# Kernel tuning notes

Measured on AMD Instinct MI355X. Metric: run time of the kernel, lower is better.

Reference implementation:

```python
import jax, jax.numpy as jnp
import numpy as np

S, B, D, H, FF = 1024, 8, 512, 8, 2048
HD = D // H
ALPHA, BETA = 0.5, 0.5
EPS = 1e-5


def setup_inputs() -> dict:
    key = jax.random.key(0)
    ks = jax.random.split(key, 12)
    rn = lambda k, sh, sc=0.02: jax.random.normal(k, sh, dtype=jnp.float32) * sc
    ln = jnp.stack([jnp.ones(D), jnp.zeros(D), jnp.ones(D), jnp.zeros(D)]).astype(jnp.float32)
    return {
        "src": rn(ks[0], (S, B, D), 1.0),
        "src_depth": rn(ks[1], (S, B, D), 1.0),
        "pos": rn(ks[2], (S, B, D), 1.0),
        "attn_w_img": rn(ks[3], (4, D, D)),
        "attn_b_img": jnp.zeros((4, D), jnp.float32),
        "attn_w_dpt": rn(ks[4], (4, D, D)),
        "attn_b_dpt": jnp.zeros((4, D), jnp.float32),
        "ffn_w1_img": rn(ks[5], (FF, D)),
        "ffn_b1_img": jnp.zeros((FF,), jnp.float32),
        "ffn_w2_img": rn(ks[6], (D, FF)),
        "ffn_b2_img": jnp.zeros((D,), jnp.float32),
        "ffn_w1_dpt": rn(ks[7], (FF, D)),
        "ffn_b1_dpt": jnp.zeros((FF,), jnp.float32),
        "ffn_w2_dpt": rn(ks[8], (D, FF)),
        "ffn_b2_dpt": jnp.zeros((D,), jnp.float32),
        "ln_img": ln,
        "ln_dpt": ln,
    }


def _layer_norm(x, g, b):
    m = jnp.mean(x, axis=-1, keepdims=True)
    v = jnp.var(x, axis=-1, keepdims=True)  # biased, matches torch LayerNorm
    return (x - m) * jax.lax.rsqrt(v + EPS) * g + b


def _heads(t, W, b):  # [B,S,D] x [D,D] -> [B,H,S,hd]  (torch Linear: y = x W^T + b)
    y = jnp.einsum('bsd,ed->bse', t, W) + b
    return y.reshape(B, S, H, HD).transpose(0, 2, 1, 3)


def _forward(src, src_depth, pos, attn_w_img, attn_b_img, attn_w_dpt, attn_b_dpt,
             ffn_w1_img, ffn_b1_img, ffn_w2_img, ffn_b2_img,
             ffn_w1_dpt, ffn_b1_dpt, ffn_w2_dpt, ffn_b2_dpt, ln_img, ln_dpt):
    # seq-first -> batch-first
    x = src.transpose(1, 0, 2)        # [B,S,D]
    xd = src_depth.transpose(1, 0, 2)
    p = pos.transpose(1, 0, 2)
    qk_in = x + p                     # img stream: q = k = src + pos
    # depth stream: pos_depth is None in layer.forward -> no pos embed
    q = _heads(qk_in, attn_w_img[0], attn_b_img[0])
    k = _heads(qk_in, attn_w_img[1], attn_b_img[1])
    v = _heads(x, attn_w_img[2], attn_b_img[2])
    qd = _heads(xd, attn_w_dpt[0], attn_b_dpt[0])
    kd = _heads(xd, attn_w_dpt[1], attn_b_dpt[1])
    vd = _heads(xd, attn_w_dpt[2], attn_b_dpt[2])
    scale = 1.0 / np.sqrt(HD).astype(np.float32)
    a_img = jax.nn.softmax(jnp.einsum('bhld,bhsd->bhls', q, k) * scale, axis=-1)
    a_dpt = jax.nn.softmax(jnp.einsum('bhld,bhsd->bhls', qd, kd) * scale, axis=-1)
    sh_img = (1.0 - ALPHA) * a_img + ALPHA * a_dpt
    sh_dpt = (1.0 - BETA) * a_dpt + BETA * a_img
    o_img = jnp.einsum('bhls,bhsd->bhld', sh_img, v).transpose(0, 2, 1, 3).reshape(B, S, D)
    o_dpt = jnp.einsum('bhls,bhsd->bhld', sh_dpt, vd).transpose(0, 2, 1, 3).reshape(B, S, D)
    o_img = jnp.einsum('bsd,ed->bse', o_img, attn_w_img[3]) + attn_b_img[3]
    o_dpt = jnp.einsum('bsd,ed->bse', o_dpt, attn_w_dpt[3]) + attn_b_dpt[3]
    # img residual + LN + FFN + LN
    x = _layer_norm(x + o_img, ln_img[0], ln_img[1])
    ff = jnp.einsum('bsf,df->bsd',
                    jax.nn.relu(jnp.einsum('bsd,fd->bsf', x, ffn_w1_img) + ffn_b1_img),
                    ffn_w2_img) + ffn_b2_img
    x = _layer_norm(x + ff, ln_img[2], ln_img[3])
    # depth residual + LN + FFN + LN
    xd = _layer_norm(xd + o_dpt, ln_dpt[0], ln_dpt[1])
    ffd = jnp.einsum('bsf,df->bsd',
                     jax.nn.relu(jnp.einsum('bsd,fd->bsf', xd, ffn_w1_dpt) + ffn_b1_dpt),
                     ffn_w2_dpt) + ffn_b2_dpt
    xd = _layer_norm(xd + ffd, ln_dpt[2], ln_dpt[3])
    return x.transpose(1, 0, 2), xd.transpose(1, 0, 2)  # back to [S,B,D]


def reference(src, src_depth, pos, attn_w_img, attn_b_img, attn_w_dpt, attn_b_dpt,
              ffn_w1_img, ffn_b1_img, ffn_w2_img, ffn_b2_img,
              ffn_w1_dpt, ffn_b1_dpt, ffn_w2_dpt, ffn_b2_dpt, ln_img, ln_dpt):
    return _forward(src, src_depth, pos, attn_w_img, attn_b_img, attn_w_dpt, attn_b_dpt,
                    ffn_w1_img, ffn_b1_img, ffn_w2_img, ffn_b2_img,
                    ffn_w1_dpt, ffn_b1_dpt, ffn_w2_dpt, ffn_b2_dpt, ln_img, ln_dpt)
```

## Files before the change

### kernel.cpp

```cpp
#include <hip/hip_runtime.h>
#include <math.h>

#define S_  1024
#define B_  8
#define D_  512
#define H_  8
#define HD_ 64
#define FF_ 2048
#define M_  8192
#define DD_ (D_ * D_)

typedef __attribute__((ext_vector_type(8))) short short8;
typedef __attribute__((ext_vector_type(4))) float f32x4;

static __device__ __forceinline__ unsigned short f2bf(float x) {
  union { float f; unsigned int u; } v; v.f = x;
  unsigned int r = v.u + 0x7fff + ((v.u >> 16) & 1);
  return (unsigned short)(r >> 16);
}
static __device__ __forceinline__ float bf2f(unsigned short x) {
  union { unsigned int u; float f; } v; v.u = ((unsigned int)x) << 16;
  return v.f;
}
static __device__ __forceinline__ unsigned int pack_bf2(float a, float b) {
  union { float f; unsigned int u; } x, y; x.f = a; y.f = b;
  return ((x.u + 0x8000u) >> 16) | ((y.u + 0x8000u) & 0xffff0000u);
}
static __device__ __forceinline__ void gl_lds16(const unsigned short* g, unsigned short* l) {
  __builtin_amdgcn_global_load_lds((__attribute__((address_space(1))) void*)(g),
                                   (__attribute__((address_space(3))) void*)(l), 16, 0, 0);
}

struct CvtJobs { const float* in[6]; unsigned short* out[6]; };
__global__ __launch_bounds__(256) void wcvt_kernel(CvtJobs j) {
  int job = blockIdx.y;
  int i = (blockIdx.x * 256 + threadIdx.x) * 4;
  float4 v = *(const float4*)(j.in[job] + i);
  unsigned short u[4] = {f2bf(v.x), f2bf(v.y), f2bf(v.z), f2bf(v.w)};
  *(uint2*)(j.out[job] + i) = *(const uint2*)u;
}

__global__ __launch_bounds__(256) void acvt_kernel(const float* __restrict__ src,
    const float* __restrict__ srcd, const float* __restrict__ pos,
    unsigned short* __restrict__ src16, unsigned short* __restrict__ srcd16,
    unsigned short* __restrict__ qkin16) {
  int job = blockIdx.y;
  int i = (blockIdx.x * 256 + threadIdx.x) * 4;
  const float* a = (job == 0) ? src : (job == 1) ? srcd : src;
  float4 v = *(const float4*)(a + i);
  if (job == 2) {
    float4 p = *(const float4*)(pos + i);
    v.x += p.x; v.y += p.y; v.z += p.z; v.w += p.w;
  }
  unsigned short* o = (job == 0) ? src16 : (job == 1) ? srcd16 : qkin16;
  unsigned short u[4] = {f2bf(v.x), f2bf(v.y), f2bf(v.z), f2bf(v.w)};
  *(uint2*)(o + i) = *(const uint2*)u;
}

static __device__ __forceinline__ void mgemm_body(
    const unsigned short* __restrict__ X, const unsigned short* __restrict__ W,
    const float* __restrict__ bias, const float* __restrict__ resf,
    const unsigned short* __restrict__ resb, unsigned short* __restrict__ Yb,
    float* __restrict__ Yf, int N, int K, int relu, int bx, int by,
    unsigned short* As, unsigned short* Bs)
{
  int tid = threadIdx.x;
  int lane = tid & 63, w = tid >> 6;
  int ml = lane & 15, g = lane >> 4;
  int wm = w >> 1, wn = w & 1;
  int m0 = by * 128, n0 = bx * 128;

  int lrow = tid >> 3;
  int lcol = ((tid & 7) ^ (lrow & 7)) * 8;
  const unsigned short* gA = X + (size_t)(m0 + lrow) * K + lcol;
  const unsigned short* gB = W + (size_t)(n0 + lrow) * K + lcol;
  unsigned short* lA = As + w * 512;
  unsigned short* lB = Bs + w * 512;

  f32x4 acc[4][4];
  #pragma unroll
  for (int i = 0; i < 4; i++)
    #pragma unroll
    for (int j = 0; j < 4; j++) acc[i][j] = (f32x4){0.f, 0.f, 0.f, 0.f};

  int NT = K >> 6;

  auto STAGE = [&](int buf, int k0) {
    const unsigned short* ga = gA + k0;
    const unsigned short* gb = gB + k0;
    unsigned short* la = lA + buf * 8192;
    unsigned short* lb = lB + buf * 8192;
    #pragma unroll
    for (int rr = 0; rr < 4; rr++) {
      gl_lds16(ga + (size_t)rr * 32 * K, la + rr * 2048);
      gl_lds16(gb + (size_t)rr * 32 * K, lb + rr * 2048);
    }
  };

  STAGE(0, 0);
  __syncthreads();

  for (int kt = 0; kt < NT; kt++) {
    int cur = kt & 1;
    if (kt + 1 < NT) STAGE(cur ^ 1, (kt + 1) * 64);

    const unsigned short* lAc = As + cur * 8192;
    const unsigned short* lBc = Bs + cur * 8192;
    #pragma unroll
    for (int ks = 0; ks < 2; ks++) {
      short8 af[4], bfr[4];
      #pragma unroll
      for (int i = 0; i < 4; i++) {
        int r = wm * 64 + i * 16 + ml;
        af[i] = *(const short8*)&lAc[r * 64 + (((ks * 4 + g) ^ (r & 7)) * 8)];
      }
      #pragma unroll
      for (int j = 0; j < 4; j++) {
        int r = wn * 64 + j * 16 + ml;
        bfr[j] = *(const short8*)&lBc[r * 64 + (((ks * 4 + g) ^ (r & 7)) * 8)];
      }
      #pragma unroll
      for (int i = 0; i < 4; i++)
        #pragma unroll
        for (int j = 0; j < 4; j++)
          acc[i][j] = __builtin_amdgcn_mfma_f32_16x16x32_bf16(af[i], bfr[j], acc[i][j], 0, 0, 0);
    }
    __syncthreads();
  }

  #pragma unroll
  for (int i = 0; i < 4; i++) {
    int grow = m0 + wm * 64 + i * 16 + g * 4;
    #pragma unroll
    for (int j = 0; j < 4; j++) {
      int gcol = n0 + wn * 64 + j * 16 + ml;
      float bv = bias[gcol];
      #pragma unroll
      for (int r = 0; r < 4; r++) {
        size_t idx = (size_t)(grow + r) * N + gcol;
        float v = acc[i][j][r] + bv;
        if (resf) v += resf[idx];
        if (resb) v += bf2f(resb[idx]);
        if (relu) v = fmaxf(v, 0.0f);
        if (Yb) Yb[idx] = f2bf(v);
        if (Yf) Yf[idx] = v;
      }
    }
  }
}

__global__ __launch_bounds__(256) void qkv_kernel(
    const unsigned short* __restrict__ qkin, const unsigned short* __restrict__ src16,
    const unsigned short* __restrict__ srcd16,
    const unsigned short* __restrict__ w_i, const unsigned short* __restrict__ w_d,
    const float* __restrict__ bA_i, const float* __restrict__ bA_d,
    unsigned short* __restrict__ qkimg, unsigned short* __restrict__ vimg,
    unsigned short* __restrict__ dptqkv)
{
  __shared__ unsigned short As[2 * 128 * 64];
  __shared__ unsigned short Bs[2 * 128 * 64];
  int bx = blockIdx.x, by = blockIdx.y;
  if (bx < 8)
    mgemm_body(qkin, w_i, bA_i, nullptr, nullptr, qkimg, nullptr, 1024, 512, 0, bx, by, As, Bs);
  else if (bx < 12)
    mgemm_body(src16, w_i + 2 * DD_, bA_i + 1024, nullptr, nullptr, vimg, nullptr, 512, 512, 0, bx - 8, by, As, Bs);
  else
    mgemm_body(srcd16, w_d, bA_d, nullptr, nullptr, dptqkv, nullptr, 1536, 512, 0, bx - 12, by, As, Bs);
}

__global__ __launch_bounds__(256) void pgemm_kernel(
    const unsigned short* __restrict__ X0, const unsigned short* __restrict__ X1,
    const unsigned short* __restrict__ W0, const unsigned short* __restrict__ W1,
    const float* __restrict__ b0, const float* __restrict__ b1,
    const float* __restrict__ rf0, const float* __restrict__ rf1,
    const unsigned short* __restrict__ rb0, const unsigned short* __restrict__ rb1,
    unsigned short* __restrict__ Y0, unsigned short* __restrict__ Y1,
    int N, int K, int relu)
{
  __shared__ unsigned short As[2 * 128 * 64];
  __shared__ unsigned short Bs[2 * 128 * 64];
  int z = blockIdx.z;
  mgemm_body(z ? X1 : X0, z ? W1 : W0, z ? b1 : b0, z ? rf1 : rf0,
             z ? rb1 : rb0, z ? Y1 : Y0, nullptr, N, K, relu,
             blockIdx.x, blockIdx.y, As, Bs);
}

__global__ __launch_bounds__(256) void vtrans_kernel(
    const unsigned short* __restrict__ v0, int ld0, unsigned short* __restrict__ vt0,
    const unsigned short* __restrict__ v1, int ld1, unsigned short* __restrict__ vt1)
{
  __shared__ unsigned short tile[64][72];
  const unsigned short* v = blockIdx.z ? v1 : v0;
  unsigned short* vt = blockIdx.z ? vt1 : vt0;
  int ld = blockIdx.z ? ld1 : ld0;
  int bh = blockIdx.y, b = bh >> 3, h = bh & 7;
  int s0 = blockIdx.x * 64;
  int tid = threadIdx.x;
  #pragma unroll
  for (int t = 0; t < 2; t++) {
    int idx = t * 256 + tid;
    int i = idx >> 3, c8 = (idx & 7) * 8;
    *(uint4*)&tile[i][c8] =
        *(const uint4*)(v + ((size_t)(s0 + i) * B_ + b) * ld + h * HD_ + c8);
  }
  __syncthreads();
  int hd = tid >> 2, j0 = (tid & 3) * 16;
  unsigned short tmp[16];
  #pragma unroll
  for (int j = 0; j < 16; j++) tmp[j] = tile[j0 + j][hd];
  unsigned short* dst = vt + ((size_t)bh * HD_ + hd) * S_ + s0 + j0;
  *(uint4*)(dst) = *(const uint4*)&tmp[0];
  *(uint4*)(dst + 8) = *(const uint4*)&tmp[8];
}

__global__ __launch_bounds__(256) void ln16_kernel(
    const unsigned short* __restrict__ X0, const unsigned short* __restrict__ X1,
    unsigned short* __restrict__ Yb0, unsigned short* __restrict__ Yb1,
    float* __restrict__ Yf0, float* __restrict__ Yf1,
    const float* __restrict__ gb0, const float* __restrict__ gb1)
{
  int row = blockIdx.x, tid = threadIdx.x;
  int strm = row >> 13, r = row & 8191;
  const unsigned short* X = strm ? X1 : X0;
  unsigned short* Yb = strm ? Yb1 : Yb0;
  float* Yf = strm ? Yf1 : Yf0;
  const float* gb = strm ? gb1 : gb0;

  ushort2 xv = *(const ushort2*)(X + (size_t)r * D_ + 2 * tid);
  float v0 = bf2f(xv.x), v1 = bf2f(xv.y);
  float s = v0 + v1, q = v0 * v0 + v1 * v1;
  #pragma unroll
  for (int msk = 1; msk < 64; msk <<= 1) {
    s += __shfl_xor(s, msk);
    q += __shfl_xor(q, msk);
  }
  __shared__ float ss[4], qs[4];
  int wid = tid >> 6;
  if ((tid & 63) == 0) { ss[wid] = s; qs[wid] = q; }
  __syncthreads();
  s = ss[0] + ss[1] + ss[2] + ss[3];
  q = qs[0] + qs[1] + qs[2] + qs[3];
  float mean = s * (1.0f / D_);
  float var  = q * (1.0f / D_) - mean * mean;
  float inv  = rsqrtf(var + 1e-5f);
  float2 gg = *(const float2*)(gb + 2 * tid);
  float2 bb = *(const float2*)(gb + 512 + 2 * tid);
  float o0 = (v0 - mean) * inv * gg.x + bb.x;
  float o1 = (v1 - mean) * inv * gg.y + bb.y;
  if (Yb) {
    unsigned int pk = pack_bf2(o0, o1);
    unsigned short u[2] = {f2bf(o0), f2bf(o1)};
    *(unsigned int*)(Yb + (size_t)r * D_ + 2 * tid) = *(const unsigned int*)u;
    (void)pk;
  }
  if (Yf) {
    float2 o; o.x = o0; o.y = o1;
    *(float2*)(Yf + (size_t)r * D_ + 2 * tid) = o;
  }
}

__global__ __launch_bounds__(256, 2) void attn_kernel(
    const unsigned short* __restrict__ Qi, const unsigned short* __restrict__ Ki, int ldi,
    const unsigned short* __restrict__ Vti,
    const unsigned short* __restrict__ Qd, const unsigned short* __restrict__ Kd, int ldd,
    const unsigned short* __restrict__ Vtd,
    unsigned short* __restrict__ oi, unsigned short* __restrict__ od)
{
  __shared__ __align__(16) unsigned short Kls[2][64 * 64];
  __shared__ __align__(16) unsigned short Vls[2][64 * 64];
  __shared__ __align__(16) unsigned short Pl[4][2][16 * 72];

  int tid = threadIdx.x;
  int bh = blockIdx.y, b = bh >> 3, h = bh & 7;
  int q0 = blockIdx.x * 128;
  int lane = tid & 63, w = tid >> 6;
  int ml = lane & 15, g = lane >> 4;
  int mx = ml & 7;

  short8 qf[2][2][2];
  #pragma unroll
  for (int t = 0; t < 2; t++) {
    size_t tok = (size_t)(q0 + w * 32 + t * 16 + ml) * B_ + b;
    const unsigned short* qa_i = Qi + tok * ldi + h * HD_ + g * 8;
    const unsigned short* qa_d = Qd + tok * ldd + h * HD_ + g * 8;
    qf[t][0][0] = *(const short8*)(qa_i);  qf[t][0][1] = *(const short8*)(qa_i + 32);
    qf[t][1][0] = *(const short8*)(qa_d);  qf[t][1][1] = *(const short8*)(qa_d + 32);
  }

  int srow = lane >> 3;
  int chg = (lane & 7) ^ srow;
  const unsigned short* gbase; size_t s1, s2; unsigned short* lbase;
  if (w == 0)      { gbase = Ki  + ((size_t)srow * B_ + b) * ldi + h * HD_ + chg * 8; s1 = (size_t)B_ * ldi; s2 = s1; lbase = &Kls[0][0]; }
  else if (w == 1) { gbase = Kd  + ((size_t)srow * B_ + b) * ldd + h * HD_ + chg * 8; s1 = (size_t)B_ * ldd; s2 = s1; lbase = &Kls[1][0]; }
  else if (w == 2) { gbase = Vti + (size_t)bh * HD_ * S_ + (size_t)srow * S_ + chg * 8; s1 = S_; s2 = 1; lbase = &Vls[0][0]; }
  else             { gbase = Vtd + (size_t)bh * HD_ * S_ + (size_t)srow * S_ + chg * 8; s1 = S_; s2 = 1; lbase = &Vls[1][0]; }

  f32x4 acc4[2][4][4];
  #pragma unroll
  for (int t = 0; t < 2; t++)
    #pragma unroll
    for (int cb = 0; cb < 4; cb++)
      #pragma unroll
      for (int n = 0; n < 4; n++) acc4[t][cb][n] = (f32x4){0.f, 0.f, 0.f, 0.f};
  float lI[2] = {0.f, 0.f}, lD[2] = {0.f, 0.f};
  const float scale = 0.125f;

  for (int kt = 0; kt < S_ / 64; kt++) {
    int k0 = kt * 64;
    __syncthreads();
    {
      const unsigned short* gp = gbase + (size_t)k0 * s2;
      #pragma unroll
      for (int rr = 0; rr < 8; rr++)
        gl_lds16(gp + (size_t)rr * 8 * s1, lbase + rr * 512);
    }
    __syncthreads();

    #pragma unroll
    for (int t = 0; t < 2; t++) {
      #pragma unroll
      for (int st = 0; st < 2; st++) {
        float* ls = st ? &lD[t] : &lI[t];
        const unsigned short* Kt = &Kls[st][0];
        #pragma unroll
        for (int n = 0; n < 4; n++) {
          int rbase = (n * 16 + ml) * 64;
          short8 kf0 = *(const short8*)&Kt[rbase + ((g ^ mx) * 8)];
          short8 kf1 = *(const short8*)&Kt[rbase + (((g + 4) ^ mx) * 8)];
          f32x4 a = (f32x4){0.f, 0.f, 0.f, 0.f};
          a = __builtin_amdgcn_mfma_f32_16x16x32_bf16(kf0, qf[t][st][0], a, 0, 0, 0);
          a = __builtin_amdgcn_mfma_f32_16x16x32_bf16(kf1, qf[t][st][1], a, 0, 0, 0);
          float p0 = __expf(a[0] * scale), p1 = __expf(a[1] * scale);
          float p2 = __expf(a[2] * scale), p3 = __expf(a[3] * scale);
          *ls += (p0 + p1) + (p2 + p3);
          uint2 pk; pk.x = pack_bf2(p0, p1); pk.y = pack_bf2(p2, p3);
          *(uint2*)&Pl[w][st][ml * 72 + n * 16 + g * 4] = pk;
        }
      }
      #pragma unroll
      for (int c = 0; c < 2; c++) {
        short8 pI = *(const short8*)&Pl[w][0][ml * 72 + g * 8 + c * 32];
        short8 pD = *(const short8*)&Pl[w][1][ml * 72 + g * 8 + c * 32];
        #pragma unroll
        for (int n = 0; n < 4; n++) {
          int rbase = (n * 16 + ml) * 64;
          int sc = (((g + 4 * c) ^ mx)) * 8;
          short8 vI = *(const short8*)&Vls[0][rbase + sc];
          short8 vD = *(const short8*)&Vls[1][rbase + sc];
          acc4[t][0][n] = __builtin_amdgcn_mfma_f32_16x16x32_bf16(pI, vI, acc4[t][0][n], 0, 0, 0);
          acc4[t][1][n] = __builtin_amdgcn_mfma_f32_16x16x32_bf16(pD, vI, acc4[t][1][n], 0, 0, 0);
          acc4[t][2][n] = __builtin_amdgcn_mfma_f32_16x16x32_bf16(pI, vD, acc4[t][2][n], 0, 0, 0);
          acc4[t][3][n] = __builtin_amdgcn_mfma_f32_16x16x32_bf16(pD, vD, acc4[t][3][n], 0, 0, 0);
        }
      }
    }
  }

  #pragma unroll
  for (int t = 0; t < 2; t++) {
    lI[t] += __shfl_xor(lI[t], 16);  lI[t] += __shfl_xor(lI[t], 32);
    lD[t] += __shfl_xor(lD[t], 16);  lD[t] += __shfl_xor(lD[t], 32);
  }
  #pragma unroll
  for (int t = 0; t < 2; t++) {
    float invI = 1.0f / lI[t], invD = 1.0f / lD[t];
    #pragma unroll
    for (int r = 0; r < 4; r++) {
      float iI = __shfl(invI, g * 4 + r, 16);
      float iD = __shfl(invD, g * 4 + r, 16);
      int qrow = q0 + w * 32 + t * 16 + g * 4 + r;
      size_t ob = ((size_t)qrow * B_ + b) * D_ + h * HD_;
      #pragma unroll
      for (int n = 0; n < 4; n++) {
        oi[ob + n * 16 + ml] = f2bf(0.5f * (acc4[t][0][n][r] * iI + acc4[t][1][n][r] * iD));
        od[ob + n * 16 + ml] = f2bf(0.5f * (acc4[t][3][n][r] * iD + acc4[t][2][n][r] * iI));
      }
    }
  }
}

extern "C" void kernel_launch(void* const* d_in, const int* in_sizes, int n_in,
                              void* d_out, int out_size, void* d_ws, size_t ws_size,
                              hipStream_t stream) {
  const float* src  = (const float*)d_in[0];
  const float* srcd = (const float*)d_in[1];
  const float* pos  = (const float*)d_in[2];
  const float* wA_i = (const float*)d_in[3];
  const float* bA_i = (const float*)d_in[4];
  const float* wA_d = (const float*)d_in[5];
  const float* bA_d = (const float*)d_in[6];
  const float* w1_i = (const float*)d_in[7];
  const float* b1_i = (const float*)d_in[8];
  const float* w2_i = (const float*)d_in[9];
  const float* b2_i = (const float*)d_in[10];
  const float* w1_d = (const float*)d_in[11];
  const float* b1_d = (const float*)d_in[12];
  const float* w2_d = (const float*)d_in[13];
  const float* b2_d = (const float*)d_in[14];
  const float* ln_i = (const float*)d_in[15];
  const float* ln_d = (const float*)d_in[16];

  float* out = (float*)d_out;
  unsigned short* u = (unsigned short*)d_ws;
  const size_t T4 = (size_t)M_ * D_;
  const size_t WSZ = (size_t)FF_ * D_;

  unsigned short* src16  = u;
  unsigned short* srcd16 = u + T4;
  unsigned short* qkimg  = u + 2 * T4;
  unsigned short* vimg   = u + 4 * T4;
  unsigned short* dptqkv = u + 5 * T4;
  unsigned short* w_i16  = u + 8 * T4;
  unsigned short* w_d16  = w_i16 + WSZ;
  unsigned short* w1i16  = w_d16 + WSZ;
  unsigned short* w2i16  = w1i16 + WSZ;
  unsigned short* w1d16  = w2i16 + WSZ;
  unsigned short* w2d16  = w1d16 + WSZ;
  unsigned short* t16_i  = w2d16 + WSZ;
  unsigned short* t16_d  = t16_i + T4;
  unsigned short* x16_i  = t16_d + T4;
  unsigned short* x16_d  = x16_i + T4;
  unsigned short* vt_i   = src16;
  unsigned short* vt_d   = srcd16;
  unsigned short* h16_i  = u;
  unsigned short* h16_d  = u + 4 * T4;
  unsigned short* qkin16 = (unsigned short*)out;
  unsigned short* oi16   = (unsigned short*)out;
  unsigned short* od16   = (unsigned short*)out + T4;

  dim3 blk(256);

  CvtJobs cj;
  cj.in[0] = wA_i; cj.out[0] = w_i16;
  cj.in[1] = wA_d; cj.out[1] = w_d16;
  cj.in[2] = w1_i; cj.out[2] = w1i16;
  cj.in[3] = w2_i; cj.out[3] = w2i16;
  cj.in[4] = w1_d; cj.out[4] = w1d16;
  cj.in[5] = w2_d; cj.out[5] = w2d16;
  wcvt_kernel<<<dim3(1024, 6), blk, 0, stream>>>(cj);
  acvt_kernel<<<dim3(4096, 3), blk, 0, stream>>>(src, srcd, pos, src16, srcd16, qkin16);

  qkv_kernel<<<dim3(24, 64), blk, 0, stream>>>(qkin16, src16, srcd16, w_i16, w_d16,
                                               bA_i, bA_d, qkimg, vimg, dptqkv);
  vtrans_kernel<<<dim3(16, 64, 2), blk, 0, stream>>>(vimg, 512, vt_i, dptqkv + 1024, 1536, vt_d);

  attn_kernel<<<dim3(S_ / 128, B_ * H_), blk, 0, stream>>>(
      qkimg, qkimg + 512, 1024, vt_i, dptqkv, dptqkv + 512, 1536, vt_d, oi16, od16);

  pgemm_kernel<<<dim3(4, 64, 2), blk, 0, stream>>>(
      oi16, od16, w_i16 + 3 * DD_, w_d16 + 3 * DD_, bA_i + 1536, bA_d + 1536,
      src, srcd, nullptr, nullptr, t16_i, t16_d, 512, 512, 0);
  ln16_kernel<<<2 * M_, blk, 0, stream>>>(t16_i, t16_d, x16_i, x16_d,
                                          nullptr, nullptr, ln_i, ln_d);
  pgemm_kernel<<<dim3(16, 64, 2), blk, 0, stream>>>(
      x16_i, x16_d, w1i16, w1d16, b1_i, b1_d,
      nullptr, nullptr, nullptr, nullptr, h16_i, h16_d, 2048, 512, 1);
  pgemm_kernel<<<dim3(4, 64, 2), blk, 0, stream>>>(
      h16_i, h16_d, w2i16, w2d16, b2_i, b2_d,
      nullptr, nullptr, x16_i, x16_d, t16_i, t16_d, 512, 2048, 0);
  ln16_kernel<<<2 * M_, blk, 0, stream>>>(t16_i, t16_d, nullptr, nullptr,
                                          out, out + T4, ln_i + 2 * D_, ln_d + 2 * D_);
}
```

Measured before the change: 452.8 us.

## Deepen GEMM global-to-LDS prefetch with explicit vmcnt waits and split barriers

Restructures the GEMM main loop into a deeper software pipeline. Two K tiles are staged up front. Each iteration waits on vmcnt for only the current tile, loads all fragments for both k-substeps into registers, then issues a barrier. It then refills the just-consumed LDS buffer with tile kt+2 before running the MFMAs, so global loads overlap compute for longer. The cost is more live fragment registers, and correctness now depends on the hand-counted vmcnt(8) matching the 8 async loads per stage.

```diff
diff --git a/kernel.cpp b/kernel.cpp
--- a/kernel.cpp
+++ b/kernel.cpp
@@ -85,9 +85,9 @@
 
   int NT = K >> 6;
 
-  auto STAGE = [&](int buf, int k0) {
-    const unsigned short* ga = gA + k0;
-    const unsigned short* gb = gB + k0;
+  auto STAGE = [&](int buf, int kt) {
+    const unsigned short* ga = gA + kt * 64;
+    const unsigned short* gb = gB + kt * 64;
     unsigned short* la = lA + buf * 8192;
     unsigned short* lb = lB + buf * 8192;
     #pragma unroll
@@ -98,34 +98,47 @@
   };
 
   STAGE(0, 0);
-  __syncthreads();
+  if (NT > 1) STAGE(1, 1);
 
   for (int kt = 0; kt < NT; kt++) {
     int cur = kt & 1;
-    if (kt + 1 < NT) STAGE(cur ^ 1, (kt + 1) * 64);
+    if (kt + 1 < NT) {
+      asm volatile("s_waitcnt vmcnt(8)" ::: "memory");
+    } else {
+      asm volatile("s_waitcnt vmcnt(0)" ::: "memory");
+    }
+    __builtin_amdgcn_sched_barrier(0);
+    __builtin_amdgcn_s_barrier();
 
     const unsigned short* lAc = As + cur * 8192;
     const unsigned short* lBc = Bs + cur * 8192;
+    short8 af[2][4], bfr[2][4];
     #pragma unroll
     for (int ks = 0; ks < 2; ks++) {
-      short8 af[4], bfr[4];
       #pragma unroll
       for (int i = 0; i < 4; i++) {
         int r = wm * 64 + i * 16 + ml;
-        af[i] = *(const short8*)&lAc[r * 64 + (((ks * 4 + g) ^ (r & 7)) * 8)];
+        af[ks][i] = *(const short8*)&lAc[r * 64 + (((ks * 4 + g) ^ (r & 7)) * 8)];
       }
       #pragma unroll
       for (int j = 0; j < 4; j++) {
         int r = wn * 64 + j * 16 + ml;
-        bfr[j] = *(const short8*)&lBc[r * 64 + (((ks * 4 + g) ^ (r & 7)) * 8)];
-      }
+        bfr[ks][j] = *(const short8*)&lBc[r * 64 + (((ks * 4 + g) ^ (r & 7)) * 8)];
+      }
+    }
+    asm volatile("s_waitcnt lgkmcnt(0)" ::: "memory");
+    __builtin_amdgcn_sched_barrier(0);
+    __builtin_amdgcn_s_barrier();
+    if (kt + 2 < NT) STAGE(cur, kt + 2);
+    __builtin_amdgcn_sched_barrier(0);
+
+    #pragma unroll
+    for (int ks = 0; ks < 2; ks++)
       #pragma unroll
       for (int i = 0; i < 4; i++)
         #pragma unroll
         for (int j = 0; j < 4; j++)
-          acc[i][j] = __builtin_amdgcn_mfma_f32_16x16x32_bf16(af[i], bfr[j], acc[i][j], 0, 0, 0);
-    }
-    __syncthreads();
+          acc[i][j] = __builtin_amdgcn_mfma_f32_16x16x32_bf16(af[ks][i], bfr[ks][j], acc[i][j], 0, 0, 0);
   }
 
   #pragma unroll
```

New measurement: 459.2 us. Within noise of the previous version (+1.4%).
